# Optimization experiments

Hardware: AMD Instinct MI355X
Metric: run time of the kernel (lower is better)

## Reference

```python
import jax, jax.numpy as jnp
import numpy as np

NUM_HEADS = 16
D_MODEL = 1024
NEG_INF = -1e30


def setup_inputs() -> dict:
    key = jax.random.key(0)
    ks = jax.random.split(key, 7)
    B, S, D = 2, 2048, D_MODEL
    scale = 1.0 / np.sqrt(D)
    return {
        "queries": jax.random.normal(ks[0], (B, S, D), dtype=jnp.float32),
        "keys": jax.random.normal(ks[1], (B, S, D), dtype=jnp.float32),
        "values": jax.random.normal(ks[2], (B, S, D), dtype=jnp.float32),
        "Wq": jax.random.normal(ks[3], (D, D), dtype=jnp.float32) * scale,
        "Wk": jax.random.normal(ks[4], (D, D), dtype=jnp.float32) * scale,
        "Wv": jax.random.normal(ks[5], (D, D), dtype=jnp.float32) * scale,
        "Wo": jax.random.normal(ks[6], (D, D), dtype=jnp.float32) * scale,
    }


def _split_heads(x, h):
    # [B, S, D] -> [B, h, S, D/h]
    B, S, D = x.shape
    return x.reshape(B, S, h, D // h).transpose(0, 2, 1, 3)


def reference(queries, keys, values, Wq, Wk, Wv, Wo):
    h = NUM_HEADS
    q = _split_heads(queries @ Wq, h)  # [B, h, S, dh]
    k = _split_heads(keys @ Wk, h)
    v = _split_heads(values @ Wv, h)
    dh = q.shape[-1]
    scores = jnp.einsum("bhqd,bhkd->bhqk", q, k) / jnp.sqrt(jnp.float32(dh))
    # original quirk: exactly-zero scores are masked to -1e30 before softmax
    scores = jnp.where(scores == 0, NEG_INF, scores)
    attn = jax.nn.softmax(scores, axis=-1)
    out = jnp.einsum("bhqk,bhkd->bhqd", attn, v)  # [B, h, S, dh]
    B, _, S, _ = out.shape
    out = out.transpose(0, 2, 1, 3).reshape(B, S, h * dh)
    return out @ Wo
```

## Files before the change

kernel.cpp:

```cpp
#include <hip/hip_runtime.h>

typedef unsigned short u16;
typedef short bf16x8 __attribute__((ext_vector_type(8)));
typedef float f32x4 __attribute__((ext_vector_type(4)));
typedef float f32x16 __attribute__((ext_vector_type(16)));

namespace {

constexpr int kB = 2, kS = 2048, kD = 1024, kH = 16, kDh = 64;
constexpr float kC2 = 0.125f * 1.44269504088896341f;

__device__ inline u16 f32_bf16(float f) {
    unsigned u = __float_as_uint(f);
    u += 0x7FFFu + ((u >> 16) & 1u);
    return (u16)(u >> 16);
}

__device__ inline u16 f32_bf16_fast(float f) {
    return (u16)((__float_as_uint(f) + 0x8000u) >> 16);
}

__device__ inline float fast_exp2(float x) {
    float r;
    asm("v_exp_f32 %0, %1" : "=v"(r) : "v"(x));
    return r;
}

__device__ inline void gl_lds16(const void* g, void* l) {
    __builtin_amdgcn_global_load_lds(
        (const __attribute__((address_space(1))) void*)g,
        (__attribute__((address_space(3))) void*)l, 16, 0, 0);
}

__device__ inline int swz8(int l) {
    return ((l & 3) ^ ((l >> 2) & 3) ^ ((l >> 4) & 3)) * 8;
}

__global__ __launch_bounds__(256) void prep(
    const float* __restrict__ s0, const float* __restrict__ s1,
    const float* __restrict__ s2,
    u16* __restrict__ d0, u16* __restrict__ d1, u16* __restrict__ d2,
    const float* __restrict__ W0, const float* __restrict__ W1,
    const float* __restrict__ W2, const float* __restrict__ W3,
    u16* __restrict__ T0, u16* __restrict__ T1,
    u16* __restrict__ T2, u16* __restrict__ T3)
{
    const int y = blockIdx.y;
    if (y < 3) {
        const float* src = y == 0 ? s0 : (y == 1 ? s1 : s2);
        u16* dst = y == 0 ? d0 : (y == 1 ? d1 : d2);
        const int i = blockIdx.x * 256 + threadIdx.x;
        const float4* s4 = (const float4*)src;
        float4 a = s4[2 * i], b = s4[2 * i + 1];
        uint4 o;
        o.x = (unsigned)f32_bf16(a.x) | ((unsigned)f32_bf16(a.y) << 16);
        o.y = (unsigned)f32_bf16(a.z) | ((unsigned)f32_bf16(a.w) << 16);
        o.z = (unsigned)f32_bf16(b.x) | ((unsigned)f32_bf16(b.y) << 16);
        o.w = (unsigned)f32_bf16(b.z) | ((unsigned)f32_bf16(b.w) << 16);
        ((uint4*)dst)[i] = o;
        return;
    }
    if (blockIdx.x >= 256) return;
    const int z = y - 3;
    const float* W = z == 0 ? W0 : (z == 1 ? W1 : (z == 2 ? W2 : W3));
    u16* Wt = z == 0 ? T0 : (z == 1 ? T1 : (z == 2 ? T2 : T3));
    const float sc = (z == 0) ? kC2 : 1.0f;

    __shared__ __attribute__((aligned(16))) u16 T[64][65];
    const int t = threadIdx.x;
    const int n0 = (blockIdx.x & 15) * 64, k0 = (blockIdx.x >> 4) * 64;
    const int r = t >> 4, c4 = (t & 15) * 4;
#pragma unroll
    for (int it = 0; it < 4; ++it) {
        const int rr = r + 16 * it;
        float4 v = *(const float4*)(W + (size_t)(k0 + rr) * kD + n0 + c4);
        T[rr][c4 + 0] = f32_bf16(v.x * sc);
        T[rr][c4 + 1] = f32_bf16(v.y * sc);
        T[rr][c4 + 2] = f32_bf16(v.z * sc);
        T[rr][c4 + 3] = f32_bf16(v.w * sc);
    }
    __syncthreads();
#pragma unroll
    for (int it = 0; it < 4; ++it) {
        const int nn = r + 16 * it;
        uint2 pk;
        pk.x = (unsigned)T[c4 + 0][nn] | ((unsigned)T[c4 + 1][nn] << 16);
        pk.y = (unsigned)T[c4 + 2][nn] | ((unsigned)T[c4 + 3][nn] << 16);
        *(uint2*)(Wt + (size_t)(n0 + nn) * kD + k0 + c4) = pk;
    }
}

__global__ __launch_bounds__(256) void vtrans(
    const u16* __restrict__ V, u16* __restrict__ Vt)
{
    __shared__ __attribute__((aligned(16))) u16 T[64][65];
    const int t = threadIdx.x;
    const int s0 = blockIdx.x * 64;
    const int bh = blockIdx.y, b = bh >> 4, h = bh & 15;
    const int rr = t >> 3, c0 = (t & 7) * 8;
    union { u16 u[8]; uint4 v4; } buf;
#pragma unroll
    for (int p = 0; p < 2; ++p) {
        const int s = rr + 32 * p;
        buf.v4 = *(const uint4*)(V + (size_t)(b * kS + s0 + s) * kD + h * kDh + c0);
#pragma unroll
        for (int i = 0; i < 8; ++i) T[c0 + i][s] = buf.u[i];
    }
    __syncthreads();
#pragma unroll
    for (int p = 0; p < 2; ++p) {
        const int d = rr + 32 * p;
#pragma unroll
        for (int i = 0; i < 8; ++i) buf.u[i] = T[d][c0 + i];
        *(uint4*)(Vt + (size_t)(bh * kDh + d) * kS + s0 + c0) = buf.v4;
    }
}

template <bool F32OUT>
__device__ inline void gemm128_body(
    const u16* __restrict__ A, const u16* __restrict__ Wt,
    void* __restrict__ Cout, int M, int N, int K, int bx, int by)
{
    __shared__ __attribute__((aligned(16))) u16 As[128 * 32];
    __shared__ __attribute__((aligned(16))) u16 Bs[128 * 32];
    const int t = threadIdx.x, w = t >> 6, l = t & 63;
    const int quad = l >> 4, c = l & 15;
    const int wm = w >> 1, wn = w & 1;
    const int m0 = by * 128, n0 = bx * 128;
    const int lr = l >> 2, lc = swz8(l);
    const int xc = ((quad ^ (c & 3) ^ ((c >> 2) & 3))) * 8;

    const u16* ga0 = A  + (size_t)(m0 + w * 32 + lr) * K + lc;
    const u16* ga1 = A  + (size_t)(m0 + w * 32 + 16 + lr) * K + lc;
    const u16* gb0 = Wt + (size_t)(n0 + w * 32 + lr) * K + lc;
    const u16* gb1 = Wt + (size_t)(n0 + w * 32 + 16 + lr) * K + lc;
    u16* la0 = &As[(w * 32) * 32];
    u16* la1 = &As[(w * 32 + 16) * 32];
    u16* lb0 = &Bs[(w * 32) * 32];
    u16* lb1 = &Bs[(w * 32 + 16) * 32];

    f32x4 acc[4][4];
#pragma unroll
    for (int mi = 0; mi < 4; ++mi)
#pragma unroll
        for (int nj = 0; nj < 4; ++nj) acc[mi][nj] = 0;

    for (int k0 = 0; k0 < K; k0 += 32) {
        gl_lds16(ga0 + k0, la0);
        gl_lds16(ga1 + k0, la1);
        gl_lds16(gb0 + k0, lb0);
        gl_lds16(gb1 + k0, lb1);
        __syncthreads();
        bf16x8 af[4], bf[4];
#pragma unroll
        for (int mi = 0; mi < 4; ++mi)
            af[mi] = *(const bf16x8*)&As[(wm * 64 + mi * 16 + c) * 32 + xc];
#pragma unroll
        for (int nj = 0; nj < 4; ++nj)
            bf[nj] = *(const bf16x8*)&Bs[(wn * 64 + nj * 16 + c) * 32 + xc];
#pragma unroll
        for (int mi = 0; mi < 4; ++mi)
#pragma unroll
            for (int nj = 0; nj < 4; ++nj)
                acc[mi][nj] = __builtin_amdgcn_mfma_f32_16x16x32_bf16(
                    af[mi], bf[nj], acc[mi][nj], 0, 0, 0);
        __syncthreads();
    }

#pragma unroll
    for (int mi = 0; mi < 4; ++mi)
#pragma unroll
        for (int nj = 0; nj < 4; ++nj)
#pragma unroll
            for (int r = 0; r < 4; ++r) {
                const size_t row = m0 + wm * 64 + mi * 16 + quad * 4 + r;
                const size_t col = n0 + wn * 64 + nj * 16 + c;
                if (F32OUT)
                    ((float*)Cout)[row * N + col] = acc[mi][nj][r];
                else
                    ((u16*)Cout)[row * N + col] = f32_bf16(acc[mi][nj][r]);
            }
}

__global__ __launch_bounds__(256) void gemm_qkv(
    const u16* __restrict__ A0, const u16* __restrict__ A1,
    const u16* __restrict__ A2,
    const u16* __restrict__ W0, const u16* __restrict__ W1,
    const u16* __restrict__ W2,
    u16* __restrict__ C0, u16* __restrict__ C1, u16* __restrict__ C2)
{
    const int z = blockIdx.z;
    const u16* A  = z == 0 ? A0 : (z == 1 ? A1 : A2);
    const u16* Wt = z == 0 ? W0 : (z == 1 ? W1 : W2);
    u16* C = z == 0 ? C0 : (z == 1 ? C1 : C2);
    gemm128_body<false>(A, Wt, C, kB * kS, kD, kD, blockIdx.x, blockIdx.y);
}

__global__ __launch_bounds__(256) void gemm_out(
    const u16* __restrict__ A, const u16* __restrict__ Wt,
    float* __restrict__ C)
{
    __shared__ __attribute__((aligned(16))) u16 As[64 * 32];
    __shared__ __attribute__((aligned(16))) u16 Bs[128 * 32];
    const int N = kD, K = kD;
    const int t = threadIdx.x, w = t >> 6, l = t & 63;
    const int quad = l >> 4, c = l & 15;
    const int wm = w >> 1, wn = w & 1;
    const int m0 = blockIdx.y * 64, n0 = blockIdx.x * 128;
    const int lr = l >> 2, lc = swz8(l);
    const int xc = ((quad ^ (c & 3) ^ ((c >> 2) & 3))) * 8;

    const u16* ga  = A  + (size_t)(m0 + w * 16 + lr) * K + lc;
    const u16* gb0 = Wt + (size_t)(n0 + w * 16 + lr) * K + lc;
    const u16* gb1 = Wt + (size_t)(n0 + 64 + w * 16 + lr) * K + lc;
    u16* la  = &As[(w * 16) * 32];
    u16* lb0 = &Bs[(w * 16) * 32];
    u16* lb1 = &Bs[(64 + w * 16) * 32];

    f32x4 acc[2][4];
#pragma unroll
    for (int mi = 0; mi < 2; ++mi)
#pragma unroll
        for (int nj = 0; nj < 4; ++nj) acc[mi][nj] = 0;

    for (int k0 = 0; k0 < K; k0 += 32) {
        gl_lds16(ga + k0, la);
        gl_lds16(gb0 + k0, lb0);
        gl_lds16(gb1 + k0, lb1);
        __syncthreads();
        bf16x8 af[2], bf[4];
#pragma unroll
        for (int mi = 0; mi < 2; ++mi)
            af[mi] = *(const bf16x8*)&As[(wm * 32 + mi * 16 + c) * 32 + xc];
#pragma unroll
        for (int nj = 0; nj < 4; ++nj)
            bf[nj] = *(const bf16x8*)&Bs[(wn * 64 + nj * 16 + c) * 32 + xc];
#pragma unroll
        for (int mi = 0; mi < 2; ++mi)
#pragma unroll
            for (int nj = 0; nj < 4; ++nj)
                acc[mi][nj] = __builtin_amdgcn_mfma_f32_16x16x32_bf16(
                    af[mi], bf[nj], acc[mi][nj], 0, 0, 0);
        __syncthreads();
    }

#pragma unroll
    for (int mi = 0; mi < 2; ++mi)
#pragma unroll
        for (int nj = 0; nj < 4; ++nj)
#pragma unroll
            for (int r = 0; r < 4; ++r) {
                const size_t row = m0 + wm * 32 + mi * 16 + quad * 4 + r;
                const size_t col = n0 + wn * 64 + nj * 16 + c;
                C[row * N + col] = acc[mi][nj][r];
            }
}

__global__ __launch_bounds__(256) void attn(
    const u16* __restrict__ Q, const u16* __restrict__ K,
    const u16* __restrict__ Vt, u16* __restrict__ AO)
{
    __shared__ __attribute__((aligned(16))) u16 KsL[64 * 64];
    __shared__ __attribute__((aligned(16))) u16 VtL[64 * 64];
    __shared__ __attribute__((aligned(16))) u16 Qs[4 * 32 * 64];
    __shared__ __attribute__((aligned(16))) u16 Ps[4 * 32 * 64];

    const int t = threadIdx.x, w = t >> 6, l = t & 63;
    const int half = l >> 5, m = l & 31;
    const int q0 = blockIdx.x * 128;
    const int bh = blockIdx.y, b = bh >> 4, h = bh & 15;
    const int sl = l >> 3;
    const int sc = (l & 7) ^ sl;

    const size_t qbase = (size_t)(b * kS + q0 + w * 32) * kD + h * kDh;
#pragma unroll
    for (int i = 0; i < 4; ++i)
        gl_lds16(Q + qbase + (size_t)(i * 8 + sl) * kD + sc * 8,
                 &Qs[w * 2048 + i * 512]);
    __syncthreads();

    bf16x8 qf[4];
#pragma unroll
    for (int ch = 0; ch < 4; ++ch)
        qf[ch] = *(const bf16x8*)
            &Qs[w * 2048 + m * 64 + ((2 * ch + half) ^ (m & 7)) * 8];

    bf16x8 ones;
#pragma unroll
    for (int i = 0; i < 8; ++i) ones[i] = (short)0x3F80;

    f32x16 o0 = 0, o1 = 0, ol = 0;

    const size_t kbase = (size_t)(b * kS) * kD + h * kDh;
    const size_t vbase = (size_t)bh * kDh * kS;

    for (int kt = 0; kt < kS / 64; ++kt) {
#pragma unroll
        for (int i = 0; i < 2; ++i) {
            const int R0 = w * 16 + i * 8;
            gl_lds16(K + kbase + (size_t)(kt * 64 + R0 + sl) * kD + sc * 8,
                     &KsL[R0 * 64]);
            gl_lds16(Vt + vbase + (size_t)(R0 + sl) * kS + kt * 64 + sc * 8,
                     &VtL[R0 * 64]);
        }
        __syncthreads();

        f32x16 s0 = 0, s1 = 0;
#pragma unroll
        for (int ch = 0; ch < 4; ++ch) {
            const int xo = ((2 * ch + half) ^ (m & 7)) * 8;
            const bf16x8 kf0 = *(const bf16x8*)&KsL[(m) * 64 + xo];
            const bf16x8 kf1 = *(const bf16x8*)&KsL[(32 + m) * 64 + xo];
            s0 = __builtin_amdgcn_mfma_f32_32x32x16_bf16(qf[ch], kf0, s0, 0, 0, 0);
            s1 = __builtin_amdgcn_mfma_f32_32x32x16_bf16(qf[ch], kf1, s1, 0, 0, 0);
        }

#pragma unroll
        for (int reg = 0; reg < 16; ++reg) {
            const int qrow = (reg & 3) + 8 * (reg >> 2) + 4 * half;
            const int base = w * 2048 + qrow * 64;
            const int sw = (qrow & 7);
            {
                const int key = m;
                Ps[base + ((key >> 3) ^ sw) * 8 + (key & 7)] =
                    f32_bf16_fast(fast_exp2(s0[reg]));
            }
            {
                const int key = 32 + m;
                Ps[base + ((key >> 3) ^ sw) * 8 + (key & 7)] =
                    f32_bf16_fast(fast_exp2(s1[reg]));
            }
        }

#pragma unroll
        for (int ch = 0; ch < 4; ++ch) {
            const int xo = ((2 * ch + half) ^ (m & 7)) * 8;
            const bf16x8 pf = *(const bf16x8*)&Ps[w * 2048 + m * 64 + xo];
            const bf16x8 vf0 = *(const bf16x8*)&VtL[(m) * 64 + xo];
            const bf16x8 vf1 = *(const bf16x8*)&VtL[(32 + m) * 64 + xo];
            o0 = __builtin_amdgcn_mfma_f32_32x32x16_bf16(pf, vf0, o0, 0, 0, 0);
            o1 = __builtin_amdgcn_mfma_f32_32x32x16_bf16(pf, vf1, o1, 0, 0, 0);
            ol = __builtin_amdgcn_mfma_f32_32x32x16_bf16(pf, ones, ol, 0, 0, 0);
        }
        __syncthreads();
    }

    const size_t obase = (size_t)(b * kS + q0 + w * 32) * kD + h * kDh;
#pragma unroll
    for (int reg = 0; reg < 16; ++reg) {
        const int qrow = (reg & 3) + 8 * (reg >> 2) + 4 * half;
        const float inv = 1.0f / ol[reg];
        AO[obase + (size_t)qrow * kD + m]      = f32_bf16(o0[reg] * inv);
        AO[obase + (size_t)qrow * kD + 32 + m] = f32_bf16(o1[reg] * inv);
    }
}

}

extern "C" void kernel_launch(void* const* d_in, const int* in_sizes, int n_in,
                              void* d_out, int out_size, void* d_ws, size_t ws_size,
                              hipStream_t stream)
{
    const float* q_in = (const float*)d_in[0];
    const float* k_in = (const float*)d_in[1];
    const float* v_in = (const float*)d_in[2];
    const float* Wq   = (const float*)d_in[3];
    const float* Wk   = (const float*)d_in[4];
    const float* Wv   = (const float*)d_in[5];
    const float* Wo   = (const float*)d_in[6];

    u16* ws = (u16*)d_ws;
    const size_t M1 = 1u << 20;
    u16* xq  = ws;
    u16* xk  = ws + 4 * M1;
    u16* xv  = ws + 8 * M1;
    u16* Wtq = ws + 12 * M1;
    u16* Wtk = ws + 13 * M1;
    u16* Wtv = ws + 14 * M1;
    u16* Wto = ws + 15 * M1;
    u16* Qp  = ws + 16 * M1;
    u16* Kp  = ws + 20 * M1;
    u16* Vp  = ws + 24 * M1;
    u16* AO  = ws + 28 * M1;
    u16* Vtg = xq;

    hipLaunchKernelGGL(prep, dim3(2048, 7), dim3(256), 0, stream,
                       q_in, k_in, v_in, xq, xk, xv,
                       Wq, Wk, Wv, Wo, Wtq, Wtk, Wtv, Wto);

    hipLaunchKernelGGL(gemm_qkv, dim3(8, 32, 3), dim3(256), 0, stream,
                       xq, xk, xv, Wtq, Wtk, Wtv, Qp, Kp, Vp);

    hipLaunchKernelGGL(vtrans, dim3(32, 32), dim3(256), 0, stream, Vp, Vtg);

    hipLaunchKernelGGL(attn, dim3(16, 32), dim3(256), 0, stream, Qp, Kp, Vtg, AO);

    hipLaunchKernelGGL(gemm_out, dim3(8, 64), dim3(256), 0, stream,
                       AO, Wto, (float*)d_out);
}
```

Measured before the change: 231.9 us.

## Double-buffer K/V tiles in LDS to overlap loads with attention compute

The attention kernel now keeps two LDS buffers for the K and V^T tiles. The next tile is issued to one buffer while the current tile is computed from the other. The loop is unrolled by two with ping-pong buffers, so there is one barrier per tile instead of two. This aims to hide global-to-LDS latency behind the MFMA and exp work, at the cost of 16 KB more LDS per block, which could lower occupancy.

```diff
diff --git a/kernel.cpp b/kernel.cpp
--- a/kernel.cpp
+++ b/kernel.cpp
@@ -260,8 +260,10 @@
     const u16* __restrict__ Q, const u16* __restrict__ K,
     const u16* __restrict__ Vt, u16* __restrict__ AO)
 {
-    __shared__ __attribute__((aligned(16))) u16 KsL[64 * 64];
-    __shared__ __attribute__((aligned(16))) u16 VtL[64 * 64];
+    __shared__ __attribute__((aligned(16))) u16 KsA[64 * 64];
+    __shared__ __attribute__((aligned(16))) u16 KsB[64 * 64];
+    __shared__ __attribute__((aligned(16))) u16 VtA[64 * 64];
+    __shared__ __attribute__((aligned(16))) u16 VtB[64 * 64];
     __shared__ __attribute__((aligned(16))) u16 Qs[4 * 32 * 64];
     __shared__ __attribute__((aligned(16))) u16 Ps[4 * 32 * 64];
 
@@ -272,11 +274,26 @@
     const int sl = l >> 3;
     const int sc = (l & 7) ^ sl;
 
+    const size_t kbase = (size_t)(b * kS) * kD + h * kDh;
+    const size_t vbase = (size_t)bh * kDh * kS;
     const size_t qbase = (size_t)(b * kS + q0 + w * 32) * kD + h * kDh;
+
+    auto stage = [&](int kt, u16* KsP, u16* VtP) {
+#pragma unroll
+        for (int i = 0; i < 2; ++i) {
+            const int R0 = w * 16 + i * 8;
+            gl_lds16(K + kbase + (size_t)(kt * 64 + R0 + sl) * kD + sc * 8,
+                     &KsP[R0 * 64]);
+            gl_lds16(Vt + vbase + (size_t)(R0 + sl) * kS + kt * 64 + sc * 8,
+                     &VtP[R0 * 64]);
+        }
+    };
+
 #pragma unroll
     for (int i = 0; i < 4; ++i)
         gl_lds16(Q + qbase + (size_t)(i * 8 + sl) * kD + sc * 8,
                  &Qs[w * 2048 + i * 512]);
+    stage(0, KsA, VtA);
     __syncthreads();
 
     bf16x8 qf[4];
@@ -291,30 +308,16 @@
 
     f32x16 o0 = 0, o1 = 0, ol = 0;
 
-    const size_t kbase = (size_t)(b * kS) * kD + h * kDh;
-    const size_t vbase = (size_t)bh * kDh * kS;
-
-    for (int kt = 0; kt < kS / 64; ++kt) {
-#pragma unroll
-        for (int i = 0; i < 2; ++i) {
-            const int R0 = w * 16 + i * 8;
-            gl_lds16(K + kbase + (size_t)(kt * 64 + R0 + sl) * kD + sc * 8,
-                     &KsL[R0 * 64]);
-            gl_lds16(Vt + vbase + (size_t)(R0 + sl) * kS + kt * 64 + sc * 8,
-                     &VtL[R0 * 64]);
-        }
-        __syncthreads();
-
+    auto compute = [&](const u16* KsP, const u16* VtP) {
         f32x16 s0 = 0, s1 = 0;
 #pragma unroll
         for (int ch = 0; ch < 4; ++ch) {
             const int xo = ((2 * ch + half) ^ (m & 7)) * 8;
-            const bf16x8 kf0 = *(const bf16x8*)&KsL[(m) * 64 + xo];
-            const bf16x8 kf1 = *(const bf16x8*)&KsL[(32 + m) * 64 + xo];
+            const bf16x8 kf0 = *(const bf16x8*)&KsP[(m) * 64 + xo];
+            const bf16x8 kf1 = *(const bf16x8*)&KsP[(32 + m) * 64 + xo];
             s0 = __builtin_amdgcn_mfma_f32_32x32x16_bf16(qf[ch], kf0, s0, 0, 0, 0);
             s1 = __builtin_amdgcn_mfma_f32_32x32x16_bf16(qf[ch], kf1, s1, 0, 0, 0);
         }
-
 #pragma unroll
         for (int reg = 0; reg < 16; ++reg) {
             const int qrow = (reg & 3) + 8 * (reg >> 2) + 4 * half;
@@ -331,17 +334,26 @@
                     f32_bf16_fast(fast_exp2(s1[reg]));
             }
         }
-
 #pragma unroll
         for (int ch = 0; ch < 4; ++ch) {
             const int xo = ((2 * ch + half) ^ (m & 7)) * 8;
             const bf16x8 pf = *(const bf16x8*)&Ps[w * 2048 + m * 64 + xo];
-            const bf16x8 vf0 = *(const bf16x8*)&VtL[(m) * 64 + xo];
-            const bf16x8 vf1 = *(const bf16x8*)&VtL[(32 + m) * 64 + xo];
+            const bf16x8 vf0 = *(const bf16x8*)&VtP[(m) * 64 + xo];
+            const bf16x8 vf1 = *(const bf16x8*)&VtP[(32 + m) * 64 + xo];
             o0 = __builtin_amdgcn_mfma_f32_32x32x16_bf16(pf, vf0, o0, 0, 0, 0);
             o1 = __builtin_amdgcn_mfma_f32_32x32x16_bf16(pf, vf1, o1, 0, 0, 0);
             ol = __builtin_amdgcn_mfma_f32_32x32x16_bf16(pf, ones, ol, 0, 0, 0);
         }
+    };
+
+    constexpr int NT = kS / 64;
+#pragma unroll 1
+    for (int kt = 0; kt < NT; kt += 2) {
+        if (kt + 1 < NT) stage(kt + 1, KsB, VtB);
+        compute(KsA, VtA);
+        __syncthreads();
+        if (kt + 2 < NT) stage(kt + 2, KsA, VtA);
+        compute(KsB, VtB);
         __syncthreads();
     }
 
```

New measurement: 223.4 us. 1.04x faster.
